# Kernel optimization log

Measured on AMD Instinct MI355X. Metric: run time of the kernel, lower is better.

Reference implementation:

```python
import jax, jax.numpy as jnp
import numpy as np

EPS = 1e-6
B, T, E, H = 2, 512, 1024, 256
NUM_BLOCK = 12


def normalize(x):
    # RMS-style normalization over the feature dim (no learned affine)
    return x * jax.lax.rsqrt(jnp.mean(x * x, axis=-1, keepdims=True) + EPS)


def bar_quadratic_causal(a, b):
    # y_i = (1/i) * sum_{j<=i} relu(a_i + b_j)   (causal prefix mean of pairwise relation)
    # a, b: [B, T, H]
    Tn = a.shape[1]
    pair = jax.nn.relu(a[:, :, None, :] + b[:, None, :, :])  # [B, T(i), T(j), H]
    mask = jnp.tril(jnp.ones((Tn, Tn), dtype=a.dtype))        # causal j<=i
    s = jnp.einsum('bijh,ij->bih', pair, mask)
    counts = jnp.arange(1, Tn + 1, dtype=a.dtype)[None, :, None]
    return s / counts


def setup_inputs() -> dict:
    key = jax.random.key(0)
    k0, k1, k2, k3 = jax.random.split(key, 4)
    x = jax.random.normal(k0, (B, T, E), dtype=jnp.float32)
    w1 = jax.random.normal(k1, (E, H), dtype=jnp.float32) * 0.02
    b1 = jnp.zeros((H,), dtype=jnp.float32)
    w2 = jax.random.normal(k2, (E, H), dtype=jnp.float32) * 0.02
    b2 = jnp.zeros((H,), dtype=jnp.float32)
    w3 = jax.random.normal(k3, (H, E), dtype=jnp.float32) * (0.02 / np.sqrt(NUM_BLOCK))
    b3 = jnp.zeros((E,), dtype=jnp.float32)
    return {"x": x, "w1": w1, "b1": b1, "w2": w2, "b2": b2, "w3": w3, "b3": b3}


def reference(x, w1, b1, w2, b2, w3, b3):
    r = normalize(x)
    a = r @ w1 + b1
    b = r @ w2 + b2
    # PreNorm == 'approx': normalize a and b separately
    a = normalize(a)
    b = normalize(b)
    r = bar_quadratic_causal(a, b)
    # PostNorm == 'yes'
    r = normalize(r)
    r = r @ w3 + b3
    return x + r
```

## Files before the change

kernel.cpp:

```cpp
#include <hip/hip_runtime.h>

#define EPSF 1e-6f
#define Bsz 2
#define Tn  512
#define En  1024
#define Hn  256
#define Mtot (Bsz * Tn)
typedef unsigned short us_t;
typedef unsigned int   u32_t;

typedef __attribute__((ext_vector_type(8))) __fp16 f16x8;
typedef __attribute__((ext_vector_type(2))) __fp16 h2_t;
typedef __attribute__((ext_vector_type(8))) short  short8;
typedef __attribute__((ext_vector_type(4))) float  f32x4;
#define MFMA16(a, b, c) __builtin_amdgcn_mfma_f32_16x16x32_f16((a), (b), (c), 0, 0, 0)

#define GLOAD_LDS16(g, l) __builtin_amdgcn_global_load_lds( \
  (const __attribute__((address_space(1))) unsigned int*)(g), \
  (__attribute__((address_space(3))) unsigned int*)(l), 16, 0, 0)

__device__ __forceinline__ us_t f2h(float f) {
  __fp16 h = (__fp16)f;
  return __builtin_bit_cast(us_t, h);
}
__device__ __forceinline__ float h2f(us_t u) {
  return (float)__builtin_bit_cast(__fp16, u);
}
__device__ __forceinline__ uint2 pack4h(float a, float b, float c, float d) {
  uint2 r;
  r.x = (u32_t)f2h(a) | ((u32_t)f2h(b) << 16);
  r.y = (u32_t)f2h(c) | ((u32_t)f2h(d) << 16);
  return r;
}
__device__ __forceinline__ float block_reduce_sum_256(float v, float* smem) {
  #pragma unroll
  for (int off = 32; off > 0; off >>= 1) v += __shfl_down(v, off, 64);
  const int wave = threadIdx.x >> 6;
  if ((threadIdx.x & 63) == 0) smem[wave] = v;
  __syncthreads();
  float s = smem[0] + smem[1] + smem[2] + smem[3];
  __syncthreads();
  return s;
}

__global__ __launch_bounds__(256) void k_prep(
    const float* __restrict__ x,
    const float* __restrict__ w1, const float* __restrict__ w2,
    const float* __restrict__ w3,
    us_t* __restrict__ xb, float* __restrict__ rs,
    us_t* __restrict__ w1t, us_t* __restrict__ w2t, us_t* __restrict__ w3t)
{
  const int b = blockIdx.x, t = threadIdx.x;

  if (b < 256) {
    const int wid = t >> 6, lane = t & 63;
    const int q   = b >> 3;
    const int mt  = (b & 7) + 8 * (q & 7);
    const int row = 16 * mt + 4 * (q >> 3) + wid;
    const float4* xp = (const float4*)(x + (size_t)row * En);
    float4 v[4];
    #pragma unroll
    for (int i = 0; i < 4; ++i) v[i] = xp[lane + 64 * i];
    float ss = 0.f;
    #pragma unroll
    for (int i = 0; i < 4; ++i)
      ss += v[i].x*v[i].x + v[i].y*v[i].y + v[i].z*v[i].z + v[i].w*v[i].w;
    #pragma unroll
    for (int off = 32; off > 0; off >>= 1) ss += __shfl_xor(ss, off, 64);
    if (lane == 0) rs[row] = rsqrtf(ss * (1.0f / En) + EPSF);
    uint2* xo = (uint2*)(xb + (size_t)row * En);
    #pragma unroll
    for (int i = 0; i < 4; ++i)
      xo[lane + 64 * i] = pack4h(v[i].x, v[i].y, v[i].z, v[i].w);
    return;
  }

  __shared__ float ts[32][33];
  const int i = b - 256;
  const float* src; us_t* dst; int R, C, tr, tc;
  if (i < 256)      { src = w1; dst = w1t; R = 1024; C = 256;  tr = i >> 3;  tc = i & 7; }
  else if (i < 512) { int k = i - 256; src = w2; dst = w2t; R = 1024; C = 256; tr = k >> 3; tc = k & 7; }
  else              { int k = i - 512; src = w3; dst = w3t; R = 256; C = 1024; tr = k >> 5; tc = k & 31; }

  const int r = t >> 3, c4 = (t & 7) * 4;
  float4 v = *(const float4*)(src + (size_t)(tr * 32 + r) * C + tc * 32 + c4);
  ts[r][c4 + 0] = v.x; ts[r][c4 + 1] = v.y; ts[r][c4 + 2] = v.z; ts[r][c4 + 3] = v.w;
  __syncthreads();
  float o0 = ts[c4 + 0][r], o1 = ts[c4 + 1][r], o2 = ts[c4 + 2][r], o3 = ts[c4 + 3][r];
  *(uint2*)(dst + (size_t)(tc * 32 + r) * R + tr * 32 + c4) = pack4h(o0, o1, o2, o3);
}

__global__ __launch_bounds__(256, 4) void k_gemm(
    const us_t* __restrict__ xb,
    const us_t* __restrict__ w1t, const us_t* __restrict__ w2t,
    float* __restrict__ Praw)
{
  __shared__ us_t Bs[4][16][256];
  __shared__ float cmb[4][16][16];

  const int blk = blockIdx.x;
  const int mt = blk & 63, nt = blk >> 6;
  const int m0 = mt * 16, n0 = nt * 16;
  const int t = threadIdx.x;
  const int wid = t >> 6, lane = t & 63;
  const int lg = lane >> 4, lr = lane & 15;
  const int k0 = wid * 256;

  const us_t* ap = xb + (size_t)(m0 + lr) * En + k0 + lg * 8;
  f16x8 a[8];
  #pragma unroll
  for (int s = 0; s < 8; ++s) a[s] = *(const f16x8*)(ap + s * 32);

  const us_t* bbase = (n0 < Hn) ? (w1t + (size_t)n0 * En)
                                : (w2t + (size_t)(n0 - Hn) * En);
  #pragma unroll
  for (int i = 0; i < 8; ++i) {
    const int r   = 2 * i + (lane >> 5);
    const int c2b = ((lane & 31) * 16) ^ ((r & 7) << 4);
    const us_t* g = bbase + (size_t)r * En + k0 + (c2b >> 1);
    GLOAD_LDS16(g, &Bs[wid][2 * i][0]);
  }
  __syncthreads();

  f32x4 acc = {0.f,0.f,0.f,0.f};
  const us_t* bs = &Bs[wid][0][0];
  #pragma unroll
  for (int s = 0; s < 8; ++s) {
    const int c2 = (lg * 16 + s * 64) ^ ((lr & 7) << 4);
    f16x8 b = *(const f16x8*)(bs + lr * 256 + (c2 >> 1));
    acc = MFMA16(a[s], b, acc);
  }

  #pragma unroll
  for (int i = 0; i < 4; ++i)
    cmb[wid][lg * 4 + i][lr] = acc[i];
  __syncthreads();

  const int row = t >> 4, col = t & 15;
  float s2 = cmb[0][row][col] + cmb[1][row][col]
           + cmb[2][row][col] + cmb[3][row][col];
  Praw[(size_t)(m0 + row) * 512 + n0 + col] = s2;
}

__global__ __launch_bounds__(256) void k_norm(
    const float* __restrict__ Praw, const float* __restrict__ rs,
    const float* __restrict__ b2, us_t* __restrict__ BmT)
{
  const int blk = blockIdx.x, t = threadIdx.x;
  const int wid = t >> 6, lane = t & 63;
  const int h0 = lane * 4;

  __shared__ us_t ls[4][256];
  const int mt = blk & 63, sub = blk >> 6;
  const int r0 = 16 * mt + 4 * sub;
  const int r  = r0 + wid;

  float4 d = *(const float4*)(Praw + (size_t)r * 512 + Hn + h0);
  const float s0 = rs[r];
  float4 bv = *(const float4*)(b2 + h0);
  float vx = d.x * s0 + bv.x, vy = d.y * s0 + bv.y;
  float vz = d.z * s0 + bv.z, vw = d.w * s0 + bv.w;

  float ss = vx*vx + vy*vy + vz*vz + vw*vw;
  #pragma unroll
  for (int o2 = 32; o2 > 0; o2 >>= 1) ss += __shfl_xor(ss, o2, 64);
  const float sc = rsqrtf(ss * (1.0f / Hn) + EPSF);

  *(uint2*)&ls[wid][h0] = pack4h(vx*sc, vy*sc, vz*sc, vw*sc);
  __syncthreads();

  const int h = t;
  u32_t w0  = (u32_t)ls[0][h] | ((u32_t)ls[1][h] << 16);
  u32_t w1v = (u32_t)ls[2][h] | ((u32_t)ls[3][h] << 16);
  const int bb   = r0 >> 9;
  const int tcol = r0 & 511;
  *(uint2*)(BmT + (size_t)bb * Hn * Tn + (size_t)h * Tn + tcol) = make_uint2(w0, w1v);
}

#define JCHB 32
__global__ __launch_bounds__(256) void k_bar(
    const float* __restrict__ Praw, const float* __restrict__ rs,
    const float* __restrict__ b1,
    const us_t* __restrict__ BmT, us_t* __restrict__ Yb)
{
  __shared__ float red[4];
  const int raw = blockIdx.x;
  const int sel = (raw < 256) ? raw : (511 - raw);
  const int bb  = raw >> 8;
  const int i0  = sel * 2;
  const int h   = threadIdx.x;
  const int rg  = bb * Tn + i0;
  const size_t baseY = (size_t)bb * Tn * Hn;
  const us_t* __restrict__ bt = BmT + (size_t)bb * Hn * Tn + (size_t)h * Tn;

  const float b1h = b1[h];
  float v0 = fmaf(Praw[(size_t)rg * 512 + h],       rs[rg],     b1h);
  float v1 = fmaf(Praw[(size_t)(rg + 1) * 512 + h], rs[rg + 1], b1h);
  float ss0 = block_reduce_sum_256(v0 * v0, red);
  float ss1 = block_reduce_sum_256(v1 * v1, red);
  const float av0 = v0 * rsqrtf(ss0 * (1.0f / Hn) + EPSF);
  const float av1 = v1 * rsqrtf(ss1 * (1.0f / Hn) + EPSF);

  const __fp16 a0h = (__fp16)av0;
  const __fp16 a1h = (__fp16)av1;
  h2_t z2;  z2[0]  = (__fp16)0.f; z2[1]  = (__fp16)0.f;
  h2_t a02; a02[0] = a0h;         a02[1] = a0h;
  h2_t a12; a12[0] = a1h;         a12[1] = a1h;
  float sum0 = 0.f, sum1 = 0.f;

  const int nfull = i0 & ~(JCHB - 1);
  short8 c0[4], c1[4];

  #define LOADC(dst, jj) { _Pragma("unroll") \
    for (int q = 0; q < 4; ++q) dst[q] = *(const short8*)(bt + (jj) + q * 8); }
  #define PROCP(buf) { _Pragma("unroll") \
    for (int q = 0; q < 4; ++q) { \
      const h2_t* ph = (const h2_t*)&buf[q]; \
      h2_t p0 = z2, p1 = z2; \
      _Pragma("unroll") \
      for (int w2i = 0; w2i < 4; ++w2i) { \
        h2_t bv2 = ph[w2i]; \
        p0 += __builtin_elementwise_max(a02 + bv2, z2); \
        p1 += __builtin_elementwise_max(a12 + bv2, z2); \
      } \
      sum0 += (float)p0[0] + (float)p0[1]; \
      sum1 += (float)p1[0] + (float)p1[1]; } }

  if (nfull > 0) {
    LOADC(c0, 0);
    int j = 0;
    while (true) {
      const bool m1 = (j + JCHB     < nfull);
      const bool m2 = (j + 2 * JCHB < nfull);
      if (m1) LOADC(c1, j + JCHB);
      PROCP(c0);
      j += JCHB;
      if (!m1) break;
      if (m2) LOADC(c0, j + JCHB);
      PROCP(c1);
      j += JCHB;
      if (!m2) break;
    }
  }
  {
    short8 ct[4];
    LOADC(ct, nfull);
    const int lim = i0 - nfull;
    #pragma unroll
    for (int q = 0; q < 4; ++q)
      #pragma unroll
      for (int e = 0; e < 8; ++e) {
        const int jl = q * 8 + e;
        float bv = h2f((us_t)ct[q][e]);
        sum0 += (jl <= lim)     ? fmaxf((float)a0h + bv, 0.f) : 0.f;
        sum1 += (jl <= lim + 1) ? fmaxf((float)a1h + bv, 0.f) : 0.f;
      }
  }
  #undef LOADC
  #undef PROCP

  {
    float ss = block_reduce_sum_256(sum0 * sum0, red);
    float c  = (float)(i0 + 1);
    float sc = rsqrtf(ss * (1.0f / Hn) + EPSF * c * c);
    Yb[baseY + (size_t)i0 * Hn + h] = f2h(sum0 * sc);
  }
  {
    float ss = block_reduce_sum_256(sum1 * sum1, red);
    float c  = (float)(i0 + 2);
    float sc = rsqrtf(ss * (1.0f / Hn) + EPSF * c * c);
    Yb[baseY + (size_t)(i0 + 1) * Hn + h] = f2h(sum1 * sc);
  }
}

__global__ __launch_bounds__(256, 4) void k_out(
    const us_t* __restrict__ Yb, const us_t* __restrict__ w3t,
    const float* __restrict__ x, const float* __restrict__ b3,
    float* __restrict__ out)
{
  const int wid = threadIdx.x >> 6, lane = threadIdx.x & 63;
  const int wg = blockIdx.x * 4 + wid;
  const int nt = wg & 63, mt = wg >> 6;
  const int m0 = mt * 16, n0 = nt * 16;
  const int lg = lane >> 4, lr = lane & 15;

  const us_t* ap = Yb  + (size_t)(m0 + lr) * Hn + lg * 8;
  const us_t* bp = w3t + (size_t)(n0 + lr) * Hn + lg * 8;

  f16x8 a[8], b[8];
  #pragma unroll
  for (int s = 0; s < 8; ++s) a[s] = *(const f16x8*)(ap + s * 32);
  #pragma unroll
  for (int s = 0; s < 8; ++s) b[s] = *(const f16x8*)(bp + s * 32);

  f32x4 acc = {0.f,0.f,0.f,0.f};
  #pragma unroll
  for (int s = 0; s < 8; ++s) acc = MFMA16(a[s], b[s], acc);

  const int row = m0 + lg * 4;
  const int c = n0 + lr;
  const float bv = b3[c];
  #pragma unroll
  for (int i = 0; i < 4; ++i) {
    const size_t o = (size_t)(row + i) * En + c;
    out[o] = x[o] + acc[i] + bv;
  }
}

extern "C" void kernel_launch(void* const* d_in, const int* in_sizes, int n_in,
                              void* d_out, int out_size, void* d_ws, size_t ws_size,
                              hipStream_t stream) {
  const float* x  = (const float*)d_in[0];
  const float* w1 = (const float*)d_in[1];
  const float* b1 = (const float*)d_in[2];
  const float* w2 = (const float*)d_in[3];
  const float* b2 = (const float*)d_in[4];
  const float* w3 = (const float*)d_in[5];
  const float* b3 = (const float*)d_in[6];
  float* out = (float*)d_out;

  char* q = (char*)d_ws;
  float* Praw = (float*)q;  q += (size_t)Mtot * 512 * 4;
  us_t* xb    = (us_t*)q;   q += (size_t)Mtot * En * 2;
  us_t* w1t   = (us_t*)q;   q += (size_t)Hn * En * 2;
  us_t* w2t   = (us_t*)q;   q += (size_t)Hn * En * 2;
  us_t* w3t   = (us_t*)q;   q += (size_t)En * Hn * 2;
  us_t* BmT   = (us_t*)q;   q += (size_t)Mtot * Hn * 2;
  us_t* Yb    = (us_t*)q;   q += (size_t)Mtot * Hn * 2;
  float* rs   = (float*)q;  q += (size_t)Mtot * 4;

  k_prep<<<1024, 256, 0, stream>>>(x, w1, w2, w3, xb, rs, w1t, w2t, w3t);
  k_gemm<<<2048, 256, 0, stream>>>(xb, w1t, w2t, Praw);
  k_norm<<<256,  256, 0, stream>>>(Praw, rs, b2, BmT);
  k_bar <<<512,  256, 0, stream>>>(Praw, rs, b1, BmT, Yb);
  k_out <<<1024, 256, 0, stream>>>(Yb, w3t, x, b3, out);
}
```

Before: 46.57 us.

## Drop fp16 copy of x; convert in GEMM; one row per bar block

The prep kernel no longer writes an fp16 copy of x. It only computes the per-row rms scales, and the GEMM now loads fp32 x directly and converts it to fp16 in registers, after issuing the async weight loads to LDS. Separately, the causal bar kernel now handles one query row per block instead of two, doubling the grid to 1024 blocks with mirrored row pairing for load balance. This removes a global write and re-read of x, at the cost of the GEMM reading twice the bytes for A and the bar kernel reloading the BmT columns once per row instead of once per pair.

```diff
diff --git a/kernel.cpp b/kernel.cpp
--- a/kernel.cpp
+++ b/kernel.cpp
@@ -47,31 +47,24 @@
     const float* __restrict__ x,
     const float* __restrict__ w1, const float* __restrict__ w2,
     const float* __restrict__ w3,
-    us_t* __restrict__ xb, float* __restrict__ rs,
+    float* __restrict__ rs,
     us_t* __restrict__ w1t, us_t* __restrict__ w2t, us_t* __restrict__ w3t)
 {
   const int b = blockIdx.x, t = threadIdx.x;
 
   if (b < 256) {
     const int wid = t >> 6, lane = t & 63;
-    const int q   = b >> 3;
-    const int mt  = (b & 7) + 8 * (q & 7);
-    const int row = 16 * mt + 4 * (q >> 3) + wid;
+    const int row = b * 4 + wid;
     const float4* xp = (const float4*)(x + (size_t)row * En);
-    float4 v[4];
-    #pragma unroll
-    for (int i = 0; i < 4; ++i) v[i] = xp[lane + 64 * i];
     float ss = 0.f;
     #pragma unroll
-    for (int i = 0; i < 4; ++i)
-      ss += v[i].x*v[i].x + v[i].y*v[i].y + v[i].z*v[i].z + v[i].w*v[i].w;
+    for (int i = 0; i < 4; ++i) {
+      float4 v = xp[lane + 64 * i];
+      ss += v.x*v.x + v.y*v.y + v.z*v.z + v.w*v.w;
+    }
     #pragma unroll
     for (int off = 32; off > 0; off >>= 1) ss += __shfl_xor(ss, off, 64);
     if (lane == 0) rs[row] = rsqrtf(ss * (1.0f / En) + EPSF);
-    uint2* xo = (uint2*)(xb + (size_t)row * En);
-    #pragma unroll
-    for (int i = 0; i < 4; ++i)
-      xo[lane + 64 * i] = pack4h(v[i].x, v[i].y, v[i].z, v[i].w);
     return;
   }
 
@@ -91,7 +84,7 @@
 }
 
 __global__ __launch_bounds__(256, 4) void k_gemm(
-    const us_t* __restrict__ xb,
+    const float* __restrict__ x,
     const us_t* __restrict__ w1t, const us_t* __restrict__ w2t,
     float* __restrict__ Praw)
 {
@@ -106,11 +99,6 @@
   const int lg = lane >> 4, lr = lane & 15;
   const int k0 = wid * 256;
 
-  const us_t* ap = xb + (size_t)(m0 + lr) * En + k0 + lg * 8;
-  f16x8 a[8];
-  #pragma unroll
-  for (int s = 0; s < 8; ++s) a[s] = *(const f16x8*)(ap + s * 32);
-
   const us_t* bbase = (n0 < Hn) ? (w1t + (size_t)n0 * En)
                                 : (w2t + (size_t)(n0 - Hn) * En);
   #pragma unroll
@@ -119,6 +107,20 @@
     const int c2b = ((lane & 31) * 16) ^ ((r & 7) << 4);
     const us_t* g = bbase + (size_t)r * En + k0 + (c2b >> 1);
     GLOAD_LDS16(g, &Bs[wid][2 * i][0]);
+  }
+
+  const float* ap = x + (size_t)(m0 + lr) * En + k0 + lg * 8;
+  f16x8 a[8];
+  #pragma unroll
+  for (int s = 0; s < 8; ++s) {
+    float4 u0 = *(const float4*)(ap + s * 32);
+    float4 u1 = *(const float4*)(ap + s * 32 + 4);
+    f16x8 av;
+    av[0] = (__fp16)u0.x; av[1] = (__fp16)u0.y;
+    av[2] = (__fp16)u0.z; av[3] = (__fp16)u0.w;
+    av[4] = (__fp16)u1.x; av[5] = (__fp16)u1.y;
+    av[6] = (__fp16)u1.z; av[7] = (__fp16)u1.w;
+    a[s] = av;
   }
   __syncthreads();
 
@@ -185,30 +187,23 @@
 {
   __shared__ float red[4];
   const int raw = blockIdx.x;
-  const int sel = (raw < 256) ? raw : (511 - raw);
-  const int bb  = raw >> 8;
-  const int i0  = sel * 2;
+  const int bb  = raw >> 9;
+  const int i   = (raw < 512) ? raw : (1023 - raw);
   const int h   = threadIdx.x;
-  const int rg  = bb * Tn + i0;
+  const int rg  = bb * Tn + i;
   const size_t baseY = (size_t)bb * Tn * Hn;
   const us_t* __restrict__ bt = BmT + (size_t)bb * Hn * Tn + (size_t)h * Tn;
 
-  const float b1h = b1[h];
-  float v0 = fmaf(Praw[(size_t)rg * 512 + h],       rs[rg],     b1h);
-  float v1 = fmaf(Praw[(size_t)(rg + 1) * 512 + h], rs[rg + 1], b1h);
+  float v0 = fmaf(Praw[(size_t)rg * 512 + h], rs[rg], b1[h]);
   float ss0 = block_reduce_sum_256(v0 * v0, red);
-  float ss1 = block_reduce_sum_256(v1 * v1, red);
-  const float av0 = v0 * rsqrtf(ss0 * (1.0f / Hn) + EPSF);
-  const float av1 = v1 * rsqrtf(ss1 * (1.0f / Hn) + EPSF);
-
-  const __fp16 a0h = (__fp16)av0;
-  const __fp16 a1h = (__fp16)av1;
-  h2_t z2;  z2[0]  = (__fp16)0.f; z2[1]  = (__fp16)0.f;
-  h2_t a02; a02[0] = a0h;         a02[1] = a0h;
-  h2_t a12; a12[0] = a1h;         a12[1] = a1h;
-  float sum0 = 0.f, sum1 = 0.f;
-
-  const int nfull = i0 & ~(JCHB - 1);
+  const float av = v0 * rsqrtf(ss0 * (1.0f / Hn) + EPSF);
+
+  const __fp16 ah = (__fp16)av;
+  h2_t z2; z2[0] = (__fp16)0.f; z2[1] = (__fp16)0.f;
+  h2_t a2; a2[0] = ah;          a2[1] = ah;
+  float sum = 0.f;
+
+  const int nfull = i & ~(JCHB - 1);
   short8 c0[4], c1[4];
 
   #define LOADC(dst, jj) { _Pragma("unroll") \
@@ -216,15 +211,11 @@
   #define PROCP(buf) { _Pragma("unroll") \
     for (int q = 0; q < 4; ++q) { \
       const h2_t* ph = (const h2_t*)&buf[q]; \
-      h2_t p0 = z2, p1 = z2; \
+      h2_t p = z2; \
       _Pragma("unroll") \
-      for (int w2i = 0; w2i < 4; ++w2i) { \
-        h2_t bv2 = ph[w2i]; \
-        p0 += __builtin_elementwise_max(a02 + bv2, z2); \
-        p1 += __builtin_elementwise_max(a12 + bv2, z2); \
-      } \
-      sum0 += (float)p0[0] + (float)p0[1]; \
-      sum1 += (float)p1[0] + (float)p1[1]; } }
+      for (int w2i = 0; w2i < 4; ++w2i) \
+        p += __builtin_elementwise_max(a2 + ph[w2i], z2); \
+      sum += (float)p[0] + (float)p[1]; } }
 
   if (nfull > 0) {
     LOADC(c0, 0);
@@ -245,32 +236,24 @@
   {
     short8 ct[4];
     LOADC(ct, nfull);
-    const int lim = i0 - nfull;
+    const int lim = i - nfull;
+    const float af = (float)ah;
     #pragma unroll
     for (int q = 0; q < 4; ++q)
       #pragma unroll
       for (int e = 0; e < 8; ++e) {
         const int jl = q * 8 + e;
         float bv = h2f((us_t)ct[q][e]);
-        sum0 += (jl <= lim)     ? fmaxf((float)a0h + bv, 0.f) : 0.f;
-        sum1 += (jl <= lim + 1) ? fmaxf((float)a1h + bv, 0.f) : 0.f;
+        sum += (jl <= lim) ? fmaxf(af + bv, 0.f) : 0.f;
       }
   }
   #undef LOADC
   #undef PROCP
 
-  {
-    float ss = block_reduce_sum_256(sum0 * sum0, red);
-    float c  = (float)(i0 + 1);
-    float sc = rsqrtf(ss * (1.0f / Hn) + EPSF * c * c);
-    Yb[baseY + (size_t)i0 * Hn + h] = f2h(sum0 * sc);
-  }
-  {
-    float ss = block_reduce_sum_256(sum1 * sum1, red);
-    float c  = (float)(i0 + 2);
-    float sc = rsqrtf(ss * (1.0f / Hn) + EPSF * c * c);
-    Yb[baseY + (size_t)(i0 + 1) * Hn + h] = f2h(sum1 * sc);
-  }
+  float ssy = block_reduce_sum_256(sum * sum, red);
+  const float c = (float)(i + 1);
+  const float sc = rsqrtf(ssy * (1.0f / Hn) + EPSF * c * c);
+  Yb[baseY + (size_t)i * Hn + h] = f2h(sum * sc);
 }
 
 __global__ __launch_bounds__(256, 4) void k_out(
@@ -321,7 +304,6 @@
 
   char* q = (char*)d_ws;
   float* Praw = (float*)q;  q += (size_t)Mtot * 512 * 4;
-  us_t* xb    = (us_t*)q;   q += (size_t)Mtot * En * 2;
   us_t* w1t   = (us_t*)q;   q += (size_t)Hn * En * 2;
   us_t* w2t   = (us_t*)q;   q += (size_t)Hn * En * 2;
   us_t* w3t   = (us_t*)q;   q += (size_t)En * Hn * 2;
@@ -329,9 +311,9 @@
   us_t* Yb    = (us_t*)q;   q += (size_t)Mtot * Hn * 2;
   float* rs   = (float*)q;  q += (size_t)Mtot * 4;
 
-  k_prep<<<1024, 256, 0, stream>>>(x, w1, w2, w3, xb, rs, w1t, w2t, w3t);
-  k_gemm<<<2048, 256, 0, stream>>>(xb, w1t, w2t, Praw);
+  k_prep<<<1024, 256, 0, stream>>>(x, w1, w2, w3, rs, w1t, w2t, w3t);
+  k_gemm<<<2048, 256, 0, stream>>>(x, w1t, w2t, Praw);
   k_norm<<<256,  256, 0, stream>>>(Praw, rs, b2, BmT);
-  k_bar <<<512,  256, 0, stream>>>(Praw, rs, b1, BmT, Yb);
+  k_bar <<<1024, 256, 0, stream>>>(Praw, rs, b1, BmT, Yb);
   k_out <<<1024, 256, 0, stream>>>(Yb, w3t, x, b3, out);
 }
```

Result: slower. 58.96 us (+26.6%).
